# Kernel tuning notes

Hardware: AMD Instinct MI355X
Metric: run time of the kernel (lower is better)

The kernel has to match this reference:

```python
import jax, jax.numpy as jnp
import numpy as np

B, N, DIN, H, DOUT = 64, 32, 128, 256, 128  # batch, n_node(=seq len), din, hidden_dim, dout


def setup_inputs() -> dict:
    key = jax.random.key(0)
    ks = jax.random.split(key, 10)
    s = 1.0 / np.sqrt(H)  # PyTorch LSTM init scale
    return {
        "x": jax.random.normal(ks[0], (B, N, DIN), jnp.float32),
        "mask": jax.random.randint(ks[1], (B, N, N), 0, 2).astype(jnp.float32),
        # bidirectional LSTM params; gate order i,f,g,o; biases b_ih+b_hh fused
        "W_ih_f": jax.random.uniform(ks[2], (4 * H, DIN), jnp.float32, -s, s),
        "W_hh_f": jax.random.uniform(ks[3], (4 * H, H), jnp.float32, -s, s),
        "b_f": jax.random.uniform(ks[4], (4 * H,), jnp.float32, -s, s),
        "W_ih_r": jax.random.uniform(ks[5], (4 * H, DIN), jnp.float32, -s, s),
        "W_hh_r": jax.random.uniform(ks[6], (4 * H, H), jnp.float32, -s, s),
        "b_r": jax.random.uniform(ks[7], (4 * H,), jnp.float32, -s, s),
        "W_fc": jax.random.uniform(ks[8], (DOUT, 2 * H), jnp.float32, -s, s),
        "b_fc": jax.random.uniform(ks[9], (DOUT,), jnp.float32, -s, s),
    }


def _lstm_scan(xs, W_ih, W_hh, b, reverse=False):
    # xs: [T, BN, D] -> hidden states [T, BN, H] (outputs aligned to input order)
    BN = xs.shape[1]

    def cell(carry, x_t):
        h, c = carry
        g = x_t @ W_ih.T + h @ W_hh.T + b
        i, f, gg, o = jnp.split(g, 4, axis=-1)
        c = jax.nn.sigmoid(f) * c + jax.nn.sigmoid(i) * jnp.tanh(gg)
        h = jax.nn.sigmoid(o) * jnp.tanh(c)
        return (h, c), h

    init = (jnp.zeros((BN, H), xs.dtype), jnp.zeros((BN, H), xs.dtype))
    _, hs = jax.lax.scan(cell, init, xs, reverse=reverse)
    return hs


def reference(x, mask, W_ih_f, W_hh_f, b_f, W_ih_r, W_hh_r, b_r, W_fc, b_fc):
    Bb, Nn, D = x.shape
    # Fuse the per-node python loop: n_node masked copies as extra batch dim.
    xm = (x[:, None, :, :] * mask[:, :, :, None]).reshape(Bb * Nn, Nn, D)
    xs = jnp.transpose(xm, (1, 0, 2))  # [T, B*N, D]
    hf = _lstm_scan(xs, W_ih_f, W_hh_f, b_f, reverse=False)
    hr = _lstm_scan(xs, W_ih_r, W_hh_r, b_r, reverse=True)
    h = jnp.concatenate([hf, hr], axis=-1)  # [T, B*N, 2H]
    h = jnp.transpose(h, (1, 0, 2)).reshape(Bb, Nn, Nn, 2 * H)
    idx = jnp.arange(Nn)
    y = h[:, idx, idx, :]  # keep timestep i of the i-th masked run -> [B, N, 2H]
    return jax.nn.relu(y @ W_fc.T + b_fc)
```

## Files before the change

### kernel.cpp

```cpp
#include <hip/hip_runtime.h>
#include <math.h>

constexpr int kB    = 64;
constexpr int kN    = 32;
constexpr int kDIN  = 128;
constexpr int kH    = 256;
constexpr int kG4   = 1024;
constexpr int kDOUT = 128;
constexpr int kBN   = 2048;

typedef __attribute__((ext_vector_type(8))) short bf16x8;
typedef __attribute__((ext_vector_type(4))) float f32x4;

__device__ __forceinline__ float sigm(float x) {
    return __builtin_amdgcn_rcpf(1.0f + __expf(-x));
}
__device__ __forceinline__ float tanh_f(float x) {
    return 1.0f - 2.0f * __builtin_amdgcn_rcpf(1.0f + __expf(2.0f * x));
}

__device__ __forceinline__ short f2bf(float f) {
    union { float f; unsigned u; } v; v.f = f;
    unsigned r = v.u + 0x7fffu + ((v.u >> 16) & 1u);
    return (short)(r >> 16);
}
__device__ __forceinline__ float bf2f(short h) {
    union { unsigned u; float f; } v; v.u = ((unsigned)(unsigned short)h) << 16;
    return v.f;
}
__device__ __forceinline__ void split_bf(float f, short& hi, short& lo) {
    const short h = f2bf(f);
    hi = h;
    lo = f2bf(f - bf2f(h));
}
__device__ __forceinline__ void cvt8(const f32x4 a, const f32x4 b,
                                     bf16x8& hi, bf16x8& lo) {
    #pragma unroll
    for (int j = 0; j < 4; ++j) { short h, l; split_bf(a[j], h, l); hi[j] = h; lo[j] = l; }
    #pragma unroll
    for (int j = 0; j < 4; ++j) { short h, l; split_bf(b[j], h, l); hi[4 + j] = h; lo[4 + j] = l; }
}

__global__ __launch_bounds__(256) void prep_k(
    const float* __restrict__ Wihf, const float* __restrict__ Wihr,
    const float* __restrict__ Whhf, const float* __restrict__ Whhr,
    const float* __restrict__ Wfc,  const float* __restrict__ mask,
    float* __restrict__ mask_t,
    short* __restrict__ Wp_f,  short* __restrict__ Wp_r,
    short* __restrict__ Wihh_f, short* __restrict__ Wihl_f,
    short* __restrict__ Wihh_r, short* __restrict__ Wihl_r,
    short* __restrict__ Wfch,   short* __restrict__ Wfcl)
{
    const int bx  = blockIdx.x;
    const int tid = threadIdx.y * 32 + threadIdx.x;

    if (bx < 128) {
        const int idx = bx;
        const int dir = idx >> 6;
        const int wv  = (idx >> 3) & 7;
        const int kt  = idx & 7;
        const float* src = dir ? Whhr : Whhf;
        short* dst = (dir ? Wp_r : Wp_f) + (size_t)((wv * 8 + kt) * 8) * 512;
        for (int i = tid; i < 512; i += 256) {
            const int tau = i >> 6, lane = i & 63;
            const int qd = lane >> 4, l = lane & 15;
            const int gate = (tau >> 1) * 256 + wv * 32 + (tau & 1) * 16 + l;
            const int ks = kt * 32 + qd * 8;
            bf16x8 v;
            #pragma unroll
            for (int j = 0; j < 8; ++j) v[j] = f2bf(src[(size_t)gate * kH + ks + j]);
            *(bf16x8*)(dst + tau * 512 + lane * 8) = v;
        }
        return;
    }
    if (bx < 256) {
        const int idx = bx - 128;
        const int dir = idx >> 6;
        const int ng  = idx & 63;
        const float* src = dir ? Wihr : Wihf;
        short* dh = (dir ? Wihh_r : Wihh_f);
        short* dl = (dir ? Wihl_r : Wihl_f);
        const int kt   = tid >> 6;
        const int lane = tid & 63;
        const int qd   = lane >> 4, l = lane & 15;
        const int ks   = kt * 32 + qd * 8;
        bf16x8 vh, vl;
        #pragma unroll
        for (int j = 0; j < 8; ++j) {
            short h, lo;
            split_bf(src[(size_t)(ng * 16 + l) * kDIN + ks + j], h, lo);
            vh[j] = h; vl[j] = lo;
        }
        const size_t off = (size_t)((ng * 4 + kt) * 64 + lane) * 8;
        *(bf16x8*)(dh + off) = vh;
        *(bf16x8*)(dl + off) = vl;
        return;
    }
    if (bx < 264) {
        const int ng   = bx - 256;
        const int lane = tid & 63;
        const int qd   = lane >> 4, l = lane & 15;
        #pragma unroll
        for (int p = 0; p < 4; ++p) {
            const int kt = p * 4 + (tid >> 6);
            const int ks = kt * 32 + qd * 8;
            bf16x8 vh, vl;
            #pragma unroll
            for (int j = 0; j < 8; ++j) {
                short h, lo;
                split_bf(Wfc[(size_t)(ng * 16 + l) * (2 * kH) + ks + j], h, lo);
                vh[j] = h; vl[j] = lo;
            }
            const size_t off = (size_t)((ng * 16 + kt) * 64 + lane) * 8;
            *(bf16x8*)(Wfch + off) = vh;
            *(bf16x8*)(Wfcl + off) = vl;
        }
        return;
    }
    const int base = (bx - 264) * 8192 + tid;
    #pragma unroll
    for (int i = 0; i < 32; ++i) {
        const int idx = base + i * 256;
        const int n = idx >> 11, tt = (idx >> 6) & 31, b = idx & 63;
        mask_t[idx] = mask[(size_t)b * 1024 + n * 32 + tt];
    }
}

__global__ __launch_bounds__(256)
__attribute__((amdgpu_waves_per_eu(1, 1))) void k1_xw(
    const float* __restrict__ x,
    const short* __restrict__ Wihh_f, const short* __restrict__ Wihl_f,
    const short* __restrict__ Wihh_r, const short* __restrict__ Wihl_r,
    float* __restrict__ xWP_f, float* __restrict__ xWP_r)
{
    __shared__ float xs[64][128];
    const int tid  = threadIdx.x;
    const int w    = tid >> 6;
    const int lane = tid & 63;
    const int quad = lane >> 4;
    const int l15  = lane & 15;

    const int bx   = blockIdx.x;
    const int dir  = bx >> 7;
    const int rest = bx & 127;
    const int t    = rest >> 2;
    const int nt   = rest & 3;

    const short* __restrict__ Wh = dir ? Wihh_r : Wihh_f;
    const short* __restrict__ Wl = dir ? Wihl_r : Wihl_f;
    float* __restrict__ xWP = dir ? xWP_r : xWP_f;

    #pragma unroll
    for (int p = 0; p < 8; ++p) {
        const int idx = p * 256 + tid;
        const int row = idx >> 5, c4 = idx & 31;
        *(f32x4*)&xs[row][c4 * 4] =
            *(const f32x4*)&x[((size_t)row * 32 + t) * kDIN + c4 * 4];
    }
    __syncthreads();

    bf16x8 ah[4][4], al[4][4];
    #pragma unroll
    for (int Mt = 0; Mt < 4; ++Mt)
        #pragma unroll
        for (int kt = 0; kt < 4; ++kt) {
            const f32x4 a0 = *(const f32x4*)&xs[Mt * 16 + l15][kt * 32 + quad * 8];
            const f32x4 a1 = *(const f32x4*)&xs[Mt * 16 + l15][kt * 32 + quad * 8 + 4];
            cvt8(a0, a1, ah[Mt][kt], al[Mt][kt]);
        }

    f32x4 acc[4][4];
    #pragma unroll
    for (int tau = 0; tau < 4; ++tau)
        #pragma unroll
        for (int Mt = 0; Mt < 4; ++Mt) acc[tau][Mt] = (f32x4){0.f, 0.f, 0.f, 0.f};

    #pragma unroll
    for (int kt = 0; kt < 4; ++kt) {
        bf16x8 bh[4], bl[4];
        #pragma unroll
        for (int tau = 0; tau < 4; ++tau) {
            const int g16 = nt * 16 + w * 4 + tau;
            const size_t off = (size_t)((g16 * 4 + kt) * 64 + lane) * 8;
            bh[tau] = *(const bf16x8*)(Wh + off);
            bl[tau] = *(const bf16x8*)(Wl + off);
        }
        #pragma unroll
        for (int tau = 0; tau < 4; ++tau)
            #pragma unroll
            for (int Mt = 0; Mt < 4; ++Mt) {
                acc[tau][Mt] = __builtin_amdgcn_mfma_f32_16x16x32_bf16(
                    ah[Mt][kt], bh[tau], acc[tau][Mt], 0, 0, 0);
                acc[tau][Mt] = __builtin_amdgcn_mfma_f32_16x16x32_bf16(
                    ah[Mt][kt], bl[tau], acc[tau][Mt], 0, 0, 0);
                acc[tau][Mt] = __builtin_amdgcn_mfma_f32_16x16x32_bf16(
                    al[Mt][kt], bh[tau], acc[tau][Mt], 0, 0, 0);
            }
    }

    #pragma unroll
    for (int tau = 0; tau < 4; ++tau) {
        const int g16  = nt * 16 + w * 4 + tau;
        const int wg   = (g16 >> 1) & 7;
        const int taug = (g16 >> 4) * 2 + (g16 & 1);
        #pragma unroll
        for (int Mt = 0; Mt < 4; ++Mt)
            ((f32x4*)xWP)[(size_t)(t * 4 + Mt) * 4096 + wg * 512 + taug * 64
                          + quad * 16 + l15] = acc[tau][Mt];
    }
}

__global__ __launch_bounds__(1024)
__attribute__((amdgpu_waves_per_eu(4, 4))) void k2_lstm(
    const float* __restrict__ mask_t,
    const float* __restrict__ xWP_f, const float* __restrict__ xWP_r,
    const short* __restrict__ Wp_f, const short* __restrict__ Wp_r,
    const float* __restrict__ b_f,  const float* __restrict__ b_r,
    float* __restrict__ y)
{
    constexpr int HP = 272;
    __shared__ short h_lds[2][16][HP];
    __shared__ short w_lds[16][8][512];

    const int tid  = threadIdx.x;
    const int w    = tid >> 6;
    const int lane = tid & 63;
    const int quad = lane >> 4;
    const int l15  = lane & 15;

    const int bx    = blockIdx.x;
    const int dir   = bx >> 7;
    const int rest  = bx & 127;
    const int n_seq = rest >> 2;
    const int bq    = rest & 3;

    const float* __restrict__ xWP = dir ? xWP_r : xWP_f;
    const short* __restrict__ Wp  = dir ? Wp_r  : Wp_f;
    const float* __restrict__ bb  = dir ? b_r   : b_f;

    const int wv = w >> 1;
    const int wo = w & 1;

    float bias[4];
    #pragma unroll
    for (int g = 0; g < 4; ++g)
        bias[g] = bb[g * 256 + w * 16 + l15];

    bf16x8 wreg[4][4];
    #pragma unroll
    for (int kt = 0; kt < 4; ++kt)
        #pragma unroll
        for (int g = 0; g < 4; ++g)
            wreg[kt][g] = *(const bf16x8*)(
                Wp + (size_t)((wv * 8 + kt) * 8 + g * 2 + wo) * 512 + lane * 8);

    #pragma unroll
    for (int f = 0; f < 8; ++f) {
        const int kt = 4 + (f >> 2), g = f & 3;
        *(bf16x8*)&w_lds[w][f][lane * 8] = *(const bf16x8*)(
            Wp + (size_t)((wv * 8 + kt) * 8 + g * 2 + wo) * 512 + lane * 8);
    }

    float c[4];
    #pragma unroll
    for (int i = 0; i < 4; ++i) c[i] = 0.f;

    const int nsteps = dir ? (kN - n_seq) : (n_seq + 1);
    const int t0     = dir ? (kN - 1) : 0;

    const f32x4* xWPv = (const f32x4*)xWP + (wv * 512 + wo * 64 + lane);

    f32x4 xwn[4];
    f32x4 mkn;
    {
        const f32x4* xb4 = xWPv + (size_t)(t0 * 4 + bq) * 4096;
        #pragma unroll
        for (int g = 0; g < 4; ++g) xwn[g] = xb4[g * 128];
        mkn = ((const f32x4*)mask_t)[(n_seq * 32 + t0) * 16 + bq * 4 + quad];
    }

    int zro = 0;

    int cur = 0;
    for (int it = 0; it < nsteps; ++it) {
        const int t = dir ? (kN - 1 - it) : it;

        asm volatile("" : "+v"(zro));

        f32x4 acc[4];
        #pragma unroll
        for (int g = 0; g < 4; ++g)
            #pragma unroll
            for (int r = 0; r < 4; ++r)
                acc[g][r] = fmaf(mkn[r], xwn[g][r], bias[g]);

        {
            const int tn = (it + 1 < nsteps) ? (dir ? t - 1 : t + 1) : t;
            const f32x4* xb4 = xWPv + (size_t)(tn * 4 + bq) * 4096;
            #pragma unroll
            for (int g = 0; g < 4; ++g) xwn[g] = xb4[g * 128];
            mkn = ((const f32x4*)mask_t)[(n_seq * 32 + tn) * 16 + bq * 4 + quad];
        }

        if (it > 0) {
            #pragma unroll
            for (int kt = 0; kt < 4; ++kt) {
                const bf16x8 a = *(const bf16x8*)&h_lds[cur][l15][kt * 32 + quad * 8];
                #pragma unroll
                for (int g = 0; g < 4; ++g)
                    acc[g] = __builtin_amdgcn_mfma_f32_16x16x32_bf16(
                        a, wreg[kt][g], acc[g], 0, 0, 0);
            }
            #pragma unroll
            for (int kk = 0; kk < 2; ++kk) {
                const int kt = 4 + kk;
                const bf16x8 a = *(const bf16x8*)&h_lds[cur][l15][kt * 32 + quad * 8];
                #pragma unroll
                for (int g = 0; g < 4; ++g) {
                    const bf16x8 wf = *(const bf16x8*)&w_lds[w][kk * 4 + g][lane * 8 + zro];
                    acc[g] = __builtin_amdgcn_mfma_f32_16x16x32_bf16(
                        a, wf, acc[g], 0, 0, 0);
                }
            }
            #pragma unroll
            for (int kk = 0; kk < 2; ++kk) {
                const int kt = 6 + kk;
                const bf16x8 a = *(const bf16x8*)&h_lds[cur][l15][kt * 32 + quad * 8];
                #pragma unroll
                for (int g = 0; g < 4; ++g) {
                    const bf16x8 wf = *(const bf16x8*)(
                        Wp + (size_t)((wv * 8 + kt) * 8 + g * 2 + wo) * 512
                           + lane * 8 + zro);
                    acc[g] = __builtin_amdgcn_mfma_f32_16x16x32_bf16(
                        a, wf, acc[g], 0, 0, 0);
                }
            }
        }

        const int nxt = cur ^ 1;
        const int u = w * 16 + l15;
        #pragma unroll
        for (int r = 0; r < 4; ++r) {
            const float gI = acc[0][r];
            const float gF = acc[1][r];
            const float gG = acc[2][r];
            const float gO = acc[3][r];
            const float ct = sigm(gF) * c[r] + sigm(gI) * tanh_f(gG);
            c[r] = ct;
            const float hn = sigm(gO) * tanh_f(ct);
            const int m = quad * 4 + r;
            h_lds[nxt][m][u] = f2bf(hn);
            if (it == nsteps - 1)
                y[((size_t)(bq * 16 + m) * kN + n_seq) * (2 * kH)
                  + dir * kH + u] = hn;
        }
        if (it + 1 < nsteps) __syncthreads();
        cur = nxt;
    }
}

__global__ __launch_bounds__(256) void k3_out(
    const float* __restrict__ y,
    const short* __restrict__ Wfch, const short* __restrict__ Wfcl,
    const float* __restrict__ b_fc, float* __restrict__ out)
{
    __shared__ float ys[16][512];
    const int tid  = threadIdx.x;
    const int w    = tid >> 6;
    const int lane = tid & 63;
    const int quad = lane >> 4;
    const int l15  = lane & 15;
    const int r0   = blockIdx.x * 16;

    #pragma unroll
    for (int p = 0; p < 8; ++p) {
        const int idx = p * 256 + tid;
        const int row = idx >> 7, c4 = idx & 127;
        *(f32x4*)&ys[row][c4 * 4] =
            *(const f32x4*)&y[(size_t)(r0 + row) * (2 * kH) + c4 * 4];
    }
    __syncthreads();

    f32x4 acc[2];
    acc[0] = (f32x4){0.f, 0.f, 0.f, 0.f};
    acc[1] = (f32x4){0.f, 0.f, 0.f, 0.f};

    #pragma unroll
    for (int kt = 0; kt < 16; ++kt) {
        const f32x4 a0 = *(const f32x4*)&ys[l15][kt * 32 + quad * 8];
        const f32x4 a1 = *(const f32x4*)&ys[l15][kt * 32 + quad * 8 + 4];
        bf16x8 ah, al;
        cvt8(a0, a1, ah, al);
        #pragma unroll
        for (int tau = 0; tau < 2; ++tau) {
            const int ng = w * 2 + tau;
            const size_t off = (size_t)((ng * 16 + kt) * 64 + lane) * 8;
            const bf16x8 bh = *(const bf16x8*)(Wfch + off);
            const bf16x8 bl = *(const bf16x8*)(Wfcl + off);
            acc[tau] = __builtin_amdgcn_mfma_f32_16x16x32_bf16(ah, bh, acc[tau], 0, 0, 0);
            acc[tau] = __builtin_amdgcn_mfma_f32_16x16x32_bf16(ah, bl, acc[tau], 0, 0, 0);
            acc[tau] = __builtin_amdgcn_mfma_f32_16x16x32_bf16(al, bh, acc[tau], 0, 0, 0);
        }
    }

    #pragma unroll
    for (int tau = 0; tau < 2; ++tau) {
        const int dout = (w * 2 + tau) * 16 + l15;
        const float bias = b_fc[dout];
        #pragma unroll
        for (int r = 0; r < 4; ++r)
            out[(size_t)(r0 + quad * 4 + r) * kDOUT + dout] =
                fmaxf(acc[tau][r] + bias, 0.f);
    }
}

extern "C" void kernel_launch(void* const* d_in, const int* in_sizes, int n_in,
                              void* d_out, int out_size, void* d_ws, size_t ws_size,
                              hipStream_t stream) {
    const float* x      = (const float*)d_in[0];
    const float* mask   = (const float*)d_in[1];
    const float* W_ih_f = (const float*)d_in[2];
    const float* W_hh_f = (const float*)d_in[3];
    const float* b_f    = (const float*)d_in[4];
    const float* W_ih_r = (const float*)d_in[5];
    const float* W_hh_r = (const float*)d_in[6];
    const float* b_r    = (const float*)d_in[7];
    const float* W_fc   = (const float*)d_in[8];
    const float* b_fc   = (const float*)d_in[9];
    float* out = (float*)d_out;

    float* ws     = (float*)d_ws;
    float* mask_t = ws;
    float* xWP_f  = mask_t + 65536;
    float* xWP_r  = xWP_f + 2097152;
    float* yb     = xWP_r + 2097152;
    short* Wp_f   = (short*)(yb + 1048576);
    short* Wp_r   = Wp_f + 262144;
    short* Wihh_f = Wp_r + 262144;
    short* Wihl_f = Wihh_f + 131072;
    short* Wihh_r = Wihl_f + 131072;
    short* Wihl_r = Wihh_r + 131072;
    short* Wfch   = Wihl_r + 131072;
    short* Wfcl   = Wfch + 65536;

    prep_k<<<272, dim3(32, 8), 0, stream>>>(
        W_ih_f, W_ih_r, W_hh_f, W_hh_r, W_fc, mask,
        mask_t, Wp_f, Wp_r, Wihh_f, Wihl_f, Wihh_r, Wihl_r, Wfch, Wfcl);

    k1_xw<<<256, 256, 0, stream>>>(x, Wihh_f, Wihl_f, Wihh_r, Wihl_r,
                                   xWP_f, xWP_r);
    k2_lstm<<<256, 1024, 0, stream>>>(mask_t, xWP_f, xWP_r, Wp_f, Wp_r,
                                      b_f, b_r, yb);
    k3_out<<<128, 256, 0, stream>>>(yb, Wfch, Wfcl, b_fc, out);
}
```

Before: 190.8 us.

## Halve LSTM block to 8 waves, each owning 32 hidden units

The recurrent LSTM kernel now runs with 512 threads (8 waves) per block instead of 1024. Each wave computes 8 gate tiles (two 16-unit slices across the four gates), so fewer waves share the per-step barrier. Weight residency is rebalanced: 5 k-tiles stay in registers, 2 in LDS and 1 is streamed from global memory, compared with 4/2/2 before. This trades more registers and more serial MFMA work per wave for cheaper synchronisation and fewer global weight reads per step, at some risk of register spills.

```diff
diff --git a/kernel.cpp b/kernel.cpp
--- a/kernel.cpp
+++ b/kernel.cpp
@@ -210,8 +210,8 @@
     }
 }
 
-__global__ __launch_bounds__(1024)
-__attribute__((amdgpu_waves_per_eu(4, 4))) void k2_lstm(
+__global__ __launch_bounds__(512)
+__attribute__((amdgpu_waves_per_eu(2, 2))) void k2_lstm(
     const float* __restrict__ mask_t,
     const float* __restrict__ xWP_f, const float* __restrict__ xWP_r,
     const short* __restrict__ Wp_f, const short* __restrict__ Wp_r,
@@ -220,7 +220,7 @@
 {
     constexpr int HP = 272;
     __shared__ short h_lds[2][16][HP];
-    __shared__ short w_lds[16][8][512];
+    __shared__ short w_lds[8][16][512];
 
     const int tid  = threadIdx.x;
     const int w    = tid >> 6;
@@ -238,44 +238,43 @@
     const short* __restrict__ Wp  = dir ? Wp_r  : Wp_f;
     const float* __restrict__ bb  = dir ? b_r   : b_f;
 
-    const int wv = w >> 1;
-    const int wo = w & 1;
-
-    float bias[4];
+    float bias[8];
     #pragma unroll
     for (int g = 0; g < 4; ++g)
-        bias[g] = bb[g * 256 + w * 16 + l15];
-
-    bf16x8 wreg[4][4];
-    #pragma unroll
-    for (int kt = 0; kt < 4; ++kt)
-        #pragma unroll
-        for (int g = 0; g < 4; ++g)
-            wreg[kt][g] = *(const bf16x8*)(
-                Wp + (size_t)((wv * 8 + kt) * 8 + g * 2 + wo) * 512 + lane * 8);
-
-    #pragma unroll
-    for (int f = 0; f < 8; ++f) {
-        const int kt = 4 + (f >> 2), g = f & 3;
+        #pragma unroll
+        for (int q = 0; q < 2; ++q)
+            bias[g * 2 + q] = bb[g * 256 + w * 32 + q * 16 + l15];
+
+    bf16x8 wreg[5][8];
+    #pragma unroll
+    for (int kt = 0; kt < 5; ++kt)
+        #pragma unroll
+        for (int tau = 0; tau < 8; ++tau)
+            wreg[kt][tau] = *(const bf16x8*)(
+                Wp + (size_t)((w * 8 + kt) * 8 + tau) * 512 + lane * 8);
+
+    #pragma unroll
+    for (int f = 0; f < 16; ++f) {
+        const int kt = 5 + (f >> 3), tau = f & 7;
         *(bf16x8*)&w_lds[w][f][lane * 8] = *(const bf16x8*)(
-            Wp + (size_t)((wv * 8 + kt) * 8 + g * 2 + wo) * 512 + lane * 8);
-    }
-
-    float c[4];
-    #pragma unroll
-    for (int i = 0; i < 4; ++i) c[i] = 0.f;
+            Wp + (size_t)((w * 8 + kt) * 8 + tau) * 512 + lane * 8);
+    }
+
+    float c[8];
+    #pragma unroll
+    for (int i = 0; i < 8; ++i) c[i] = 0.f;
 
     const int nsteps = dir ? (kN - n_seq) : (n_seq + 1);
     const int t0     = dir ? (kN - 1) : 0;
 
-    const f32x4* xWPv = (const f32x4*)xWP + (wv * 512 + wo * 64 + lane);
-
-    f32x4 xwn[4];
+    const f32x4* xWPv = (const f32x4*)xWP + (w * 512 + lane);
+
+    f32x4 xwn[8];
     f32x4 mkn;
     {
         const f32x4* xb4 = xWPv + (size_t)(t0 * 4 + bq) * 4096;
         #pragma unroll
-        for (int g = 0; g < 4; ++g) xwn[g] = xb4[g * 128];
+        for (int tau = 0; tau < 8; ++tau) xwn[tau] = xb4[tau * 64];
         mkn = ((const f32x4*)mask_t)[(n_seq * 32 + t0) * 16 + bq * 4 + quad];
     }
 
@@ -287,73 +286,73 @@
 
         asm volatile("" : "+v"(zro));
 
-        f32x4 acc[4];
-        #pragma unroll
-        for (int g = 0; g < 4; ++g)
+        f32x4 acc[8];
+        #pragma unroll
+        for (int tau = 0; tau < 8; ++tau)
             #pragma unroll
             for (int r = 0; r < 4; ++r)
-                acc[g][r] = fmaf(mkn[r], xwn[g][r], bias[g]);
+                acc[tau][r] = fmaf(mkn[r], xwn[tau][r], bias[tau]);
 
         {
             const int tn = (it + 1 < nsteps) ? (dir ? t - 1 : t + 1) : t;
             const f32x4* xb4 = xWPv + (size_t)(tn * 4 + bq) * 4096;
             #pragma unroll
-            for (int g = 0; g < 4; ++g) xwn[g] = xb4[g * 128];
+            for (int tau = 0; tau < 8; ++tau) xwn[tau] = xb4[tau * 64];
             mkn = ((const f32x4*)mask_t)[(n_seq * 32 + tn) * 16 + bq * 4 + quad];
         }
 
         if (it > 0) {
             #pragma unroll
-            for (int kt = 0; kt < 4; ++kt) {
+            for (int kt = 0; kt < 5; ++kt) {
                 const bf16x8 a = *(const bf16x8*)&h_lds[cur][l15][kt * 32 + quad * 8];
                 #pragma unroll
-                for (int g = 0; g < 4; ++g)
-                    acc[g] = __builtin_amdgcn_mfma_f32_16x16x32_bf16(
-                        a, wreg[kt][g], acc[g], 0, 0, 0);
+                for (int tau = 0; tau < 8; ++tau)
+                    acc[tau] = __builtin_amdgcn_mfma_f32_16x16x32_bf16(
+                        a, wreg[kt][tau], acc[tau], 0, 0, 0);
             }
             #pragma unroll
             for (int kk = 0; kk < 2; ++kk) {
-                const int kt = 4 + kk;
+                const int kt = 5 + kk;
                 const bf16x8 a = *(const bf16x8*)&h_lds[cur][l15][kt * 32 + quad * 8];
                 #pragma unroll
-                for (int g = 0; g < 4; ++g) {
-                    const bf16x8 wf = *(const bf16x8*)&w_lds[w][kk * 4 + g][lane * 8 + zro];
-                    acc[g] = __builtin_amdgcn_mfma_f32_16x16x32_bf16(
-                        a, wf, acc[g], 0, 0, 0);
+                for (int tau = 0; tau < 8; ++tau) {
+                    const bf16x8 wf = *(const bf16x8*)&w_lds[w][kk * 8 + tau][lane * 8];
+                    acc[tau] = __builtin_amdgcn_mfma_f32_16x16x32_bf16(
+                        a, wf, acc[tau], 0, 0, 0);
                 }
             }
-            #pragma unroll
-            for (int kk = 0; kk < 2; ++kk) {
-                const int kt = 6 + kk;
-                const bf16x8 a = *(const bf16x8*)&h_lds[cur][l15][kt * 32 + quad * 8];
+            {
+                const bf16x8 a = *(const bf16x8*)&h_lds[cur][l15][7 * 32 + quad * 8];
                 #pragma unroll
-                for (int g = 0; g < 4; ++g) {
+                for (int tau = 0; tau < 8; ++tau) {
                     const bf16x8 wf = *(const bf16x8*)(
-                        Wp + (size_t)((wv * 8 + kt) * 8 + g * 2 + wo) * 512
-                           + lane * 8 + zro);
-                    acc[g] = __builtin_amdgcn_mfma_f32_16x16x32_bf16(
-                        a, wf, acc[g], 0, 0, 0);
+                        Wp + (size_t)((w * 8 + 7) * 8 + tau) * 512 + lane * 8 + zro);
+                    acc[tau] = __builtin_amdgcn_mfma_f32_16x16x32_bf16(
+                        a, wf, acc[tau], 0, 0, 0);
                 }
             }
         }
 
         const int nxt = cur ^ 1;
-        const int u = w * 16 + l15;
-        #pragma unroll
-        for (int r = 0; r < 4; ++r) {
-            const float gI = acc[0][r];
-            const float gF = acc[1][r];
-            const float gG = acc[2][r];
-            const float gO = acc[3][r];
-            const float ct = sigm(gF) * c[r] + sigm(gI) * tanh_f(gG);
-            c[r] = ct;
-            const float hn = sigm(gO) * tanh_f(ct);
-            const int m = quad * 4 + r;
-            h_lds[nxt][m][u] = f2bf(hn);
-            if (it == nsteps - 1)
-                y[((size_t)(bq * 16 + m) * kN + n_seq) * (2 * kH)
-                  + dir * kH + u] = hn;
-        }
+        #pragma unroll
+        for (int q = 0; q < 2; ++q)
+            #pragma unroll
+            for (int r = 0; r < 4; ++r) {
+                const int ci = q * 4 + r;
+                const float gI = acc[0 + q][r];
+                const float gF = acc[2 + q][r];
+                const float gG = acc[4 + q][r];
+                const float gO = acc[6 + q][r];
+                const float ct = sigm(gF) * c[ci] + sigm(gI) * tanh_f(gG);
+                c[ci] = ct;
+                const float hn = sigm(gO) * tanh_f(ct);
+                const int m = quad * 4 + r;
+                const int u = w * 32 + q * 16 + l15;
+                h_lds[nxt][m][u] = f2bf(hn);
+                if (it == nsteps - 1)
+                    y[((size_t)(bq * 16 + m) * kN + n_seq) * (2 * kH)
+                      + dir * kH + u] = hn;
+            }
         if (it + 1 < nsteps) __syncthreads();
         cur = nxt;
     }
@@ -449,7 +448,7 @@
 
     k1_xw<<<256, 256, 0, stream>>>(x, Wihh_f, Wihl_f, Wihh_r, Wihl_r,
                                    xWP_f, xWP_r);
-    k2_lstm<<<256, 1024, 0, stream>>>(mask_t, xWP_f, xWP_r, Wp_f, Wp_r,
-                                      b_f, b_r, yb);
+    k2_lstm<<<256, 512, 0, stream>>>(mask_t, xWP_f, xWP_r, Wp_f, Wp_r,
+                                     b_f, b_r, yb);
     k3_out<<<128, 256, 0, stream>>>(yb, Wfch, Wfcl, b_fc, out);
 }
```

New measurement: 249.5 us. 1.31x slower.

## Pre-split x and LSTM outputs into bf16 hi/lo MFMA fragment layouts

Applied to the files above, without the earlier changes.

x is now converted once in the prep kernel into hi/lo bf16 pairs stored in MFMA A-fragment order. k1 loads these fragments straight from global memory instead of staging fp32 x in LDS and converting there. The LSTM kernel likewise writes its final hidden states as hi/lo bf16 fragments, so k3 reads them directly without an LDS tile or a conversion step. This removes LDS staging, barriers and per-block conversion work, at the cost of extra prep blocks and scattered 2-byte stores from the LSTM kernel.

```diff
diff --git a/kernel.cpp b/kernel.cpp
--- a/kernel.cpp
+++ b/kernel.cpp
@@ -33,23 +33,18 @@
     hi = h;
     lo = f2bf(f - bf2f(h));
 }
-__device__ __forceinline__ void cvt8(const f32x4 a, const f32x4 b,
-                                     bf16x8& hi, bf16x8& lo) {
-    #pragma unroll
-    for (int j = 0; j < 4; ++j) { short h, l; split_bf(a[j], h, l); hi[j] = h; lo[j] = l; }
-    #pragma unroll
-    for (int j = 0; j < 4; ++j) { short h, l; split_bf(b[j], h, l); hi[4 + j] = h; lo[4 + j] = l; }
-}
 
 __global__ __launch_bounds__(256) void prep_k(
     const float* __restrict__ Wihf, const float* __restrict__ Wihr,
     const float* __restrict__ Whhf, const float* __restrict__ Whhr,
     const float* __restrict__ Wfc,  const float* __restrict__ mask,
+    const float* __restrict__ x,
     float* __restrict__ mask_t,
     short* __restrict__ Wp_f,  short* __restrict__ Wp_r,
     short* __restrict__ Wihh_f, short* __restrict__ Wihl_f,
     short* __restrict__ Wihh_r, short* __restrict__ Wihl_r,
-    short* __restrict__ Wfch,   short* __restrict__ Wfcl)
+    short* __restrict__ Wfch,   short* __restrict__ Wfcl,
+    short* __restrict__ xPh,    short* __restrict__ xPl)
 {
     const int bx  = blockIdx.x;
     const int tid = threadIdx.y * 32 + threadIdx.x;
@@ -117,23 +112,44 @@
         }
         return;
     }
-    const int base = (bx - 264) * 8192 + tid;
-    #pragma unroll
-    for (int i = 0; i < 32; ++i) {
-        const int idx = base + i * 256;
-        const int n = idx >> 11, tt = (idx >> 6) & 31, b = idx & 63;
-        mask_t[idx] = mask[(size_t)b * 1024 + n * 32 + tt];
+    if (bx < 272) {
+        const int base = (bx - 264) * 8192 + tid;
+        #pragma unroll
+        for (int i = 0; i < 32; ++i) {
+            const int idx = base + i * 256;
+            const int n = idx >> 11, tt = (idx >> 6) & 31, b = idx & 63;
+            mask_t[idx] = mask[(size_t)b * 1024 + n * 32 + tt];
+        }
+        return;
+    }
+    {
+        const int t = bx - 272;
+        for (int i = tid; i < 1024; i += 256) {
+            const int Mt = i >> 8, kt = (i >> 6) & 3, lane = i & 63;
+            const int l15 = lane & 15, qk = lane >> 4;
+            const int b = Mt * 16 + l15;
+            const int ks = kt * 32 + qk * 8;
+            bf16x8 vh, vl;
+            #pragma unroll
+            for (int j = 0; j < 8; ++j) {
+                short h, lo;
+                split_bf(x[((size_t)b * kN + t) * kDIN + ks + j], h, lo);
+                vh[j] = h; vl[j] = lo;
+            }
+            const size_t off = (size_t)(((t * 4 + Mt) * 4 + kt) * 64 + lane) * 8;
+            *(bf16x8*)(xPh + off) = vh;
+            *(bf16x8*)(xPl + off) = vl;
+        }
     }
 }
 
 __global__ __launch_bounds__(256)
 __attribute__((amdgpu_waves_per_eu(1, 1))) void k1_xw(
-    const float* __restrict__ x,
+    const short* __restrict__ xPh, const short* __restrict__ xPl,
     const short* __restrict__ Wihh_f, const short* __restrict__ Wihl_f,
     const short* __restrict__ Wihh_r, const short* __restrict__ Wihl_r,
     float* __restrict__ xWP_f, float* __restrict__ xWP_r)
 {
-    __shared__ float xs[64][128];
     const int tid  = threadIdx.x;
     const int w    = tid >> 6;
     const int lane = tid & 63;
@@ -150,25 +166,6 @@
     const short* __restrict__ Wl = dir ? Wihl_r : Wihl_f;
     float* __restrict__ xWP = dir ? xWP_r : xWP_f;
 
-    #pragma unroll
-    for (int p = 0; p < 8; ++p) {
-        const int idx = p * 256 + tid;
-        const int row = idx >> 5, c4 = idx & 31;
-        *(f32x4*)&xs[row][c4 * 4] =
-            *(const f32x4*)&x[((size_t)row * 32 + t) * kDIN + c4 * 4];
-    }
-    __syncthreads();
-
-    bf16x8 ah[4][4], al[4][4];
-    #pragma unroll
-    for (int Mt = 0; Mt < 4; ++Mt)
-        #pragma unroll
-        for (int kt = 0; kt < 4; ++kt) {
-            const f32x4 a0 = *(const f32x4*)&xs[Mt * 16 + l15][kt * 32 + quad * 8];
-            const f32x4 a1 = *(const f32x4*)&xs[Mt * 16 + l15][kt * 32 + quad * 8 + 4];
-            cvt8(a0, a1, ah[Mt][kt], al[Mt][kt]);
-        }
-
     f32x4 acc[4][4];
     #pragma unroll
     for (int tau = 0; tau < 4; ++tau)
@@ -177,6 +174,13 @@
 
     #pragma unroll
     for (int kt = 0; kt < 4; ++kt) {
+        bf16x8 ah[4], al[4];
+        #pragma unroll
+        for (int Mt = 0; Mt < 4; ++Mt) {
+            const size_t aoff = (size_t)(((t * 4 + Mt) * 4 + kt) * 64 + lane) * 8;
+            ah[Mt] = *(const bf16x8*)(xPh + aoff);
+            al[Mt] = *(const bf16x8*)(xPl + aoff);
+        }
         bf16x8 bh[4], bl[4];
         #pragma unroll
         for (int tau = 0; tau < 4; ++tau) {
@@ -190,11 +194,11 @@
             #pragma unroll
             for (int Mt = 0; Mt < 4; ++Mt) {
                 acc[tau][Mt] = __builtin_amdgcn_mfma_f32_16x16x32_bf16(
-                    ah[Mt][kt], bh[tau], acc[tau][Mt], 0, 0, 0);
+                    ah[Mt], bh[tau], acc[tau][Mt], 0, 0, 0);
                 acc[tau][Mt] = __builtin_amdgcn_mfma_f32_16x16x32_bf16(
-                    ah[Mt][kt], bl[tau], acc[tau][Mt], 0, 0, 0);
+                    ah[Mt], bl[tau], acc[tau][Mt], 0, 0, 0);
                 acc[tau][Mt] = __builtin_amdgcn_mfma_f32_16x16x32_bf16(
-                    al[Mt][kt], bh[tau], acc[tau][Mt], 0, 0, 0);
+                    al[Mt], bh[tau], acc[tau][Mt], 0, 0, 0);
             }
     }
 
@@ -216,7 +220,7 @@
     const float* __restrict__ xWP_f, const float* __restrict__ xWP_r,
     const short* __restrict__ Wp_f, const short* __restrict__ Wp_r,
     const float* __restrict__ b_f,  const float* __restrict__ b_r,
-    float* __restrict__ y)
+    short* __restrict__ yPh, short* __restrict__ yPl)
 {
     constexpr int HP = 272;
     __shared__ short h_lds[2][16][HP];
@@ -349,10 +353,17 @@
             c[r] = ct;
             const float hn = sigm(gO) * tanh_f(ct);
             const int m = quad * 4 + r;
-            h_lds[nxt][m][u] = f2bf(hn);
-            if (it == nsteps - 1)
-                y[((size_t)(bq * 16 + m) * kN + n_seq) * (2 * kH)
-                  + dir * kH + u] = hn;
+            const short hh = f2bf(hn);
+            h_lds[nxt][m][u] = hh;
+            if (it == nsteps - 1) {
+                const int gr  = (bq * 16 + m) * kN + n_seq;
+                const int kt3 = dir * 8 + (w >> 1);
+                const int qk  = (w & 1) * 2 + (l15 >> 3);
+                const size_t off = ((size_t)((gr >> 4) * 16 + kt3) * 512)
+                                 + (size_t)((gr & 15) + 16 * qk) * 8 + (l15 & 7);
+                yPh[off] = hh;
+                yPl[off] = f2bf(hn - bf2f(hh));
+            }
         }
         if (it + 1 < nsteps) __syncthreads();
         cur = nxt;
@@ -360,11 +371,10 @@
 }
 
 __global__ __launch_bounds__(256) void k3_out(
-    const float* __restrict__ y,
+    const short* __restrict__ yPh, const short* __restrict__ yPl,
     const short* __restrict__ Wfch, const short* __restrict__ Wfcl,
     const float* __restrict__ b_fc, float* __restrict__ out)
 {
-    __shared__ float ys[16][512];
     const int tid  = threadIdx.x;
     const int w    = tid >> 6;
     const int lane = tid & 63;
@@ -372,25 +382,15 @@
     const int l15  = lane & 15;
     const int r0   = blockIdx.x * 16;
 
-    #pragma unroll
-    for (int p = 0; p < 8; ++p) {
-        const int idx = p * 256 + tid;
-        const int row = idx >> 7, c4 = idx & 127;
-        *(f32x4*)&ys[row][c4 * 4] =
-            *(const f32x4*)&y[(size_t)(r0 + row) * (2 * kH) + c4 * 4];
-    }
-    __syncthreads();
-
     f32x4 acc[2];
     acc[0] = (f32x4){0.f, 0.f, 0.f, 0.f};
     acc[1] = (f32x4){0.f, 0.f, 0.f, 0.f};
 
     #pragma unroll
     for (int kt = 0; kt < 16; ++kt) {
-        const f32x4 a0 = *(const f32x4*)&ys[l15][kt * 32 + quad * 8];
-        const f32x4 a1 = *(const f32x4*)&ys[l15][kt * 32 + quad * 8 + 4];
-        bf16x8 ah, al;
-        cvt8(a0, a1, ah, al);
+        const size_t aoff = ((size_t)(blockIdx.x * 16 + kt) * 512) + (size_t)lane * 8;
+        const bf16x8 ah = *(const bf16x8*)(yPh + aoff);
+        const bf16x8 al = *(const bf16x8*)(yPl + aoff);
         #pragma unroll
         for (int tau = 0; tau < 2; ++tau) {
             const int ng = w * 2 + tau;
@@ -433,8 +433,7 @@
     float* mask_t = ws;
     float* xWP_f  = mask_t + 65536;
     float* xWP_r  = xWP_f + 2097152;
-    float* yb     = xWP_r + 2097152;
-    short* Wp_f   = (short*)(yb + 1048576);
+    short* Wp_f   = (short*)(xWP_r + 2097152);
     short* Wp_r   = Wp_f + 262144;
     short* Wihh_f = Wp_r + 262144;
     short* Wihl_f = Wihh_f + 131072;
@@ -442,14 +441,19 @@
     short* Wihl_r = Wihh_r + 131072;
     short* Wfch   = Wihl_r + 131072;
     short* Wfcl   = Wfch + 65536;
-
-    prep_k<<<272, dim3(32, 8), 0, stream>>>(
-        W_ih_f, W_ih_r, W_hh_f, W_hh_r, W_fc, mask,
-        mask_t, Wp_f, Wp_r, Wihh_f, Wihl_f, Wihh_r, Wihl_r, Wfch, Wfcl);
-
-    k1_xw<<<256, 256, 0, stream>>>(x, Wihh_f, Wihl_f, Wihh_r, Wihl_r,
+    short* xPh    = Wfcl + 65536;
+    short* xPl    = xPh + 262144;
+    short* yPh    = xPl + 262144;
+    short* yPl    = yPh + 1048576;
+
+    prep_k<<<304, dim3(32, 8), 0, stream>>>(
+        W_ih_f, W_ih_r, W_hh_f, W_hh_r, W_fc, mask, x,
+        mask_t, Wp_f, Wp_r, Wihh_f, Wihl_f, Wihh_r, Wihl_r, Wfch, Wfcl,
+        xPh, xPl);
+
+    k1_xw<<<256, 256, 0, stream>>>(xPh, xPl, Wihh_f, Wihl_f, Wihh_r, Wihl_r,
                                    xWP_f, xWP_r);
     k2_lstm<<<256, 1024, 0, stream>>>(mask_t, xWP_f, xWP_r, Wp_f, Wp_r,
-                                      b_f, b_r, yb);
-    k3_out<<<128, 256, 0, stream>>>(yb, Wfch, Wfcl, b_fc, out);
-}
+                                      b_f, b_r, yPh, yPl);
+    k3_out<<<128, 256, 0, stream>>>(yPh, yPl, Wfch, Wfcl, b_fc, out);
+}
```

Result: slower. 199.4 us (+4.5%).
